# Kernel optimization log

Measured on AMD Instinct MI355X. Metric: run time of the kernel, lower is better.

Reference implementation:

```python
import jax, jax.numpy as jnp
import numpy as np

N_FFT = 2048
STRIDE = 512
FREQ_BINS = N_FFT  # __init__ passes freq_bins=n_fft


def _fourier_kernels():
    s = np.arange(N_FFT, dtype=np.float64)
    # scipy get_window('hann', n_fft, fftbins=True)
    win = 0.5 - 0.5 * np.cos(2.0 * np.pi * s / N_FFT)
    k = np.arange(FREQ_BINS, dtype=np.float64)
    phase = 2.0 * np.pi * np.outer(k, s) / N_FFT  # (bins, n_fft)
    wsin = (win * np.sin(phase)).astype(np.float32)
    wcos = (win * np.cos(phase)).astype(np.float32)
    return wsin, wcos


def setup_inputs() -> dict:
    key = jax.random.key(0)
    x = jax.random.normal(key, (8, 262144), dtype=jnp.float32)
    wsin, wcos = _fourier_kernels()
    return {"x": x, "wsin": jnp.asarray(wsin), "wcos": jnp.asarray(wcos)}


def reference(x, wsin, wcos):
    # center=True, pad_mode='reflect'
    xp = jnp.pad(x, ((0, 0), (N_FFT // 2, N_FFT // 2)), mode="reflect")
    num_frames = (xp.shape[1] - N_FFT) // STRIDE + 1
    # frame the signal: (batch, num_frames, n_fft)
    idx = np.arange(num_frames)[:, None] * STRIDE + np.arange(N_FFT)
    frames = xp[:, idx]
    # dense DFT as GEMM (equivalent to conv1d with sin/cos filters)
    imag = jnp.einsum("btn,kn->bkt", frames, wsin)
    real = jnp.einsum("btn,kn->bkt", frames, wcos)
    return (real, -imag)
```

## Files before the change

### kernel.cpp

```cpp
#include <hip/hip_runtime.h>
#include <hip/hip_bf16.h>
#include <stdint.h>

#define XLEN   262144
#define NT     513
#define NTP    528
#define NB     8
#define NCOL   (NB * NTP)
#define NKC4   320
#define KQ     512
#define NK     1088
#define NFFT   2048
#define OUTKT  (2048 * NT)
#define WSTR   ((size_t)NKC4 * KQ)
#define FSTR   ((size_t)NCOL * KQ)
#define PSTR   ((size_t)NKC4 * NCOL)

typedef __attribute__((ext_vector_type(8))) short short8;
typedef __attribute__((ext_vector_type(4))) short short4v;
typedef __attribute__((ext_vector_type(2))) short short2v;
typedef __attribute__((ext_vector_type(4))) float f32x4;

__device__ __forceinline__ short cvt_bf16(float f) {
  return __builtin_bit_cast(short, (__bf16)f);
}

__device__ __forceinline__ f32x4 bf4_to_f32(short4v v) {
  f32x4 o;
#pragma unroll
  for (int e = 0; e < 4; ++e) {
    uint32_t u = ((uint32_t)(uint16_t)v[e]) << 16;
    o[e] = __builtin_bit_cast(float, u);
  }
  return o;
}

__device__ __forceinline__ void gload16(const short* g, const short* l) {
  __builtin_amdgcn_global_load_lds(
      (const __attribute__((address_space(1))) void*)g,
      (__attribute__((address_space(3))) void*)l, 16, 0, 0);
}


__global__ __launch_bounds__(256) void conv_prep4(
    const float* __restrict__ x,
    const float* __restrict__ wsin, const float* __restrict__ wcos,
    short* __restrict__ wc4, short* __restrict__ ws4,
    short* __restrict__ fr4) {
  const int n0 = threadIdx.x * 8;
  const int m0 = n0 >> 2;
  if (blockIdx.x < NKC4) {
    const int row = blockIdx.x;
    short2v c[4], s[4];
    if (row <= 256) {
      const float* pc = wcos + (size_t)row * NFFT + n0;
      const float* ps = wsin + (size_t)row * NFFT + n0;
      f32x4 c0 = *(const f32x4*)pc, c1 = *(const f32x4*)(pc + 4);
      f32x4 s0 = *(const f32x4*)ps, s1 = *(const f32x4*)(ps + 4);
#pragma unroll
      for (int r = 0; r < 4; ++r) {
        c[r][0] = cvt_bf16(c0[r]); c[r][1] = cvt_bf16(c1[r]);
        s[r][0] = cvt_bf16(s0[r]); s[r][1] = cvt_bf16(s1[r]);
      }
    } else {
#pragma unroll
      for (int r = 0; r < 4; ++r) { c[r][0] = 0; c[r][1] = 0; s[r][0] = 0; s[r][1] = 0; }
    }
    const size_t o = (size_t)row * KQ + m0;
#pragma unroll
    for (int r = 0; r < 4; ++r) {
      *(short2v*)&wc4[r * WSTR + o] = c[r];
      *(short2v*)&ws4[r * WSTR + o] = s[r];
    }
  } else {
    const int j = blockIdx.x - NKC4;
    const int b = j / NTP;
    const int t = j - b * NTP;
    short2v v[4];
    if (t < NT) {
      const float* xb = x + (size_t)b * XLEN;
      const int q0 = t * 512 + n0 - 1024;
      float f[8];
      if (q0 >= 0 && q0 + 7 < XLEN) {
        *(f32x4*)(f)     = *(const f32x4*)(xb + q0);
        *(f32x4*)(f + 4) = *(const f32x4*)(xb + q0 + 4);
      } else {
#pragma unroll
        for (int e = 0; e < 8; ++e) {
          int mm = q0 + e;
          mm = (mm < 0) ? -mm : mm;
          mm = (mm >= XLEN) ? (2 * XLEN - 2 - mm) : mm;
          f[e] = xb[mm];
        }
      }
#pragma unroll
      for (int r = 0; r < 4; ++r) { v[r][0] = cvt_bf16(f[r]); v[r][1] = cvt_bf16(f[4 + r]); }
    } else {
#pragma unroll
      for (int r = 0; r < 4; ++r) { v[r][0] = 0; v[r][1] = 0; }
    }
#pragma unroll
    for (int r = 0; r < 4; ++r)
      *(short2v*)&fr4[r * FSTR + (size_t)j * KQ + m0] = v[r];
  }
}

__global__ __launch_bounds__(256, 3) void dft_gemm_split4(
    const short* __restrict__ wc4, const short* __restrict__ ws4,
    const short* __restrict__ fr4,
    short* __restrict__ pC4, short* __restrict__ pS4) {
  __shared__ short lds[16384];

  const int tid  = threadIdx.x;
  const int lane = tid & 63;
  const int wid  = tid >> 6;

  const int o   = blockIdx.x;
  const int xcd = o & 7;
  const int i   = o >> 3;
  const int wg  = ((xcd < 4) ? xcd * 83 : 332 + (xcd - 4) * 82) + i;
  const int side = wg / 165;
  const int w    = wg - side * 165;
  const int k0   = (w % 5) * 64;
  const int j0   = (w / 5) * 128;

  const short* Ac = wc4 + side * WSTR;
  const short* As = ws4 + side * WSTR;
  const short* Bf = fr4 + side * FSTR;
  short* pC = pC4 + side * PSTR;
  short* pS = pS4 + side * PSTR;

  const int wrow = (wid >> 1) * 32;
  const int wcol = (wid & 1) * 64;

  f32x4 accC[2][4], accS[2][4];
#pragma unroll
  for (int m = 0; m < 2; ++m)
#pragma unroll
    for (int n = 0; n < 4; ++n) { accC[m][n] = (f32x4)0.0f; accS[m][n] = (f32x4)0.0f; }

  const int fr_r = lane & 15;
  const int srow = lane >> 3;
  const int scol = ((lane & 7) ^ srow) * 8;

  auto stage = [&](int n0) {
#pragma unroll
    for (int i2 = 0; i2 < 8; ++i2) {
      const int q = wid * 8 + i2;
      const short* src;
      int dst;
      if (q < 8) {
        src = Ac + (size_t)(k0 + q * 8 + srow) * KQ + n0 + scol;
        dst = q * 512;
      } else if (q < 16) {
        src = As + (size_t)(k0 + (q - 8) * 8 + srow) * KQ + n0 + scol;
        dst = 4096 + (q - 8) * 512;
      } else {
        src = Bf + (size_t)(j0 + (q - 16) * 8 + srow) * KQ + n0 + scol;
        dst = 8192 + (q - 16) * 512;
      }
      gload16(src, &lds[dst]);
    }
  };

  for (int ts = 0; ts < 8; ++ts) {
    if (ts) __syncthreads();
    stage(ts * 64);
    __syncthreads();
#pragma unroll
    for (int ks = 0; ks < 2; ++ks) {
      const int cc = ks * 4 + (lane >> 4);
      short8 aC[2], aS[2], bF[4];
#pragma unroll
      for (int m = 0; m < 2; ++m) {
        const int r = wrow + m * 16 + fr_r;
        const int off = (r << 6) + ((cc ^ (r & 7)) << 3);
        aC[m] = *(const short8*)&lds[off];
        aS[m] = *(const short8*)&lds[4096 + off];
      }
#pragma unroll
      for (int n = 0; n < 4; ++n) {
        const int r = wcol + n * 16 + fr_r;
        const int off = (r << 6) + ((cc ^ (r & 7)) << 3);
        bF[n] = *(const short8*)&lds[8192 + off];
      }
#pragma unroll
      for (int m = 0; m < 2; ++m)
#pragma unroll
        for (int n = 0; n < 4; ++n) {
          accC[m][n] = __builtin_amdgcn_mfma_f32_16x16x32_bf16(aC[m], bF[n], accC[m][n], 0, 0, 0);
          accS[m][n] = __builtin_amdgcn_mfma_f32_16x16x32_bf16(aS[m], bF[n], accS[m][n], 0, 0, 0);
        }
    }
  }

#pragma unroll
  for (int m = 0; m < 2; ++m) {
    const int row = k0 + wrow + m * 16 + (lane >> 4) * 4;
#pragma unroll
    for (int n = 0; n < 4; ++n) {
      const int col = j0 + wcol + n * 16 + (lane & 15);
      const size_t base = (size_t)row * NCOL + col;
#pragma unroll
      for (int r = 0; r < 4; ++r) {
        pC[base + (size_t)r * NCOL] = cvt_bf16(accC[m][n][r]);
        pS[base + (size_t)r * NCOL] = cvt_bf16(accS[m][n][r]);
      }
    }
  }
}

__global__ __launch_bounds__(256) void combine4_kernel(
    const short* __restrict__ pC4, const short* __restrict__ pS4,
    float* __restrict__ outR, float* __restrict__ outI) {
  const int k  = blockIdx.y;
  const int jq = blockIdx.x * 256 + threadIdx.x;
  if (jq >= NCOL / 4) return;
  const int j = jq * 4;
  const int b = j / NTP;
  const int t = j - b * NTP;
  const size_t pb = (size_t)k * NCOL + j;
  f32x4 C[4], S[4];
#pragma unroll
  for (int r = 0; r < 4; ++r) {
    C[r] = bf4_to_f32(*(const short4v*)&pC4[r * PSTR + pb]);
    S[r] = bf4_to_f32(*(const short4v*)&pS4[r * PSTR + pb]);
  }
  const f32x4 CA = C[0] + C[2], CB = C[1] + C[3];
  const f32x4 CmA = C[0] - C[2], CmB = C[1] - C[3];
  const f32x4 SA = S[0] + S[2], SB = S[1] + S[3];
  const f32x4 SmA = S[0] - S[2], SmB = S[1] - S[3];

  f32x4 Cw[4], Sw[4];
  Cw[0] = CA + CB;   Sw[0] = SA + SB;
  Cw[1] = CmA - SmB; Sw[1] = SmA + CmB;
  Cw[2] = CA - CB;   Sw[2] = SA - SB;
  Cw[3] = CmA + SmB; Sw[3] = SmA - CmB;

  const size_t ob = (size_t)b * OUTKT + t;
  const bool mir = (k >= 1) && (k <= 255);
#pragma unroll
  for (int jj = 0; jj < 4; ++jj) {
    const int rowD = 512 * jj + k;
    float* rD = outR + ob + (size_t)rowD * NT;
    float* iD = outI + ob + (size_t)rowD * NT;
    const int rowM = 512 * (4 - jj) - k;
    float* rM = outR + ob + (size_t)rowM * NT;
    float* iM = outI + ob + (size_t)rowM * NT;
#pragma unroll
    for (int e = 0; e < 4; ++e) {
      if (t + e < NT) {
        rD[e] = Cw[jj][e];
        iD[e] = -Sw[jj][e];
        if (mir) { rM[e] = Cw[jj][e]; iM[e] = Sw[jj][e]; }
      }
    }
  }
}


__global__ __launch_bounds__(256) void conv_w_kernel(const float* __restrict__ wsin,
                                                     const float* __restrict__ wcos,
                                                     short* __restrict__ wc,
                                                     short* __restrict__ ws) {
  const int row = blockIdx.x;
  const int c = threadIdx.x * 8;
  const float* src = (blockIdx.y ? wsin : wcos) + (size_t)row * NFFT + c;
  short* dst = (blockIdx.y ? ws : wc) + (size_t)row * NFFT + c;
  f32x4 a = *(const f32x4*)src;
  f32x4 b = *(const f32x4*)(src + 4);
  short8 o;
#pragma unroll
  for (int j = 0; j < 4; ++j) { o[j] = cvt_bf16(a[j]); o[4 + j] = cvt_bf16(b[j]); }
  *(short8*)dst = o;
}

__global__ __launch_bounds__(256) void conv_frames_kernel(const float* __restrict__ x,
                                                          short* __restrict__ fr) {
  const int j = blockIdx.x;
  const int b = j / NTP;
  const int t = j - b * NTP;
  const int c = threadIdx.x * 8;
  short8 o;
  if (t >= NT) {
#pragma unroll
    for (int k = 0; k < 8; ++k) o[k] = 0;
  } else {
    const float* xb = x + (size_t)b * XLEN;
    const int base = t * 512 + c - 1024;
    float v[8];
    if (base >= 0 && base + 7 < XLEN) {
      *(f32x4*)(v)     = *(const f32x4*)(xb + base);
      *(f32x4*)(v + 4) = *(const f32x4*)(xb + base + 4);
    } else {
#pragma unroll
      for (int k = 0; k < 8; ++k) {
        int m = base + k;
        m = (m < 0) ? -m : m;
        m = (m >= XLEN) ? (2 * XLEN - 2 - m) : m;
        v[k] = xb[m];
      }
    }
#pragma unroll
    for (int k = 0; k < 8; ++k) o[k] = cvt_bf16(v[k]);
  }
  *(short8*)&fr[(size_t)j * NFFT + c] = o;
}

__global__ __launch_bounds__(256, 3) void dft_gemm_r4(
    const short* __restrict__ wc_bf,
    const short* __restrict__ ws_bf,
    const short* __restrict__ fr_bf,
    float* __restrict__ outR,
    float* __restrict__ outI) {
  __shared__ short lds[16384];

  const int tid  = threadIdx.x;
  const int lane = tid & 63;
  const int wid  = tid >> 6;

  const int o   = blockIdx.x;
  const int xcd = o & 7;
  const int wg  = ((xcd < 1) ? xcd * 71 : 71 + (xcd - 1) * 70) + (o >> 3);
  const int k0  = (wg % 17) * 64;
  const int j0  = (wg / 17) * 128;

  const int wrow = (wid >> 1) * 32;
  const int wcol = (wid & 1) * 64;

  f32x4 accR[2][4], accI[2][4];
#pragma unroll
  for (int m = 0; m < 2; ++m)
#pragma unroll
    for (int n = 0; n < 4; ++n) { accR[m][n] = (f32x4)0.0f; accI[m][n] = (f32x4)0.0f; }

  const int fr_r = lane & 15;
  const int srow = lane >> 3;
  const int scol = ((lane & 7) ^ srow) * 8;

  auto stage = [&](int n0) {
#pragma unroll
    for (int i = 0; i < 8; ++i) {
      const int q = wid * 8 + i;
      const short* src;
      int dst;
      if (q < 8) {
        src = wc_bf + (size_t)(k0 + q * 8 + srow) * NFFT + n0 + scol;
        dst = q * 512;
      } else if (q < 16) {
        src = ws_bf + (size_t)(k0 + (q - 8) * 8 + srow) * NFFT + n0 + scol;
        dst = 4096 + (q - 8) * 512;
      } else {
        src = fr_bf + (size_t)(j0 + (q - 16) * 8 + srow) * NFFT + n0 + scol;
        dst = 8192 + (q - 16) * 512;
      }
      gload16(src, &lds[dst]);
    }
  };

  for (int t = 0; t < 32; ++t) {
    if (t) __syncthreads();
    stage(t * 64);
    __syncthreads();
#pragma unroll
    for (int ks = 0; ks < 2; ++ks) {
      const int cc = ks * 4 + (lane >> 4);
      short8 a_c[2], a_s[2], b_f[4];
#pragma unroll
      for (int m = 0; m < 2; ++m) {
        const int r = wrow + m * 16 + fr_r;
        const int off = (r << 6) + ((cc ^ (r & 7)) << 3);
        a_c[m] = *(const short8*)&lds[off];
        a_s[m] = *(const short8*)&lds[4096 + off];
      }
#pragma unroll
      for (int n = 0; n < 4; ++n) {
        const int r = wcol + n * 16 + fr_r;
        const int off = (r << 6) + ((cc ^ (r & 7)) << 3);
        b_f[n] = *(const short8*)&lds[8192 + off];
      }
#pragma unroll
      for (int m = 0; m < 2; ++m)
#pragma unroll
        for (int n = 0; n < 4; ++n) {
          accR[m][n] = __builtin_amdgcn_mfma_f32_16x16x32_bf16(a_c[m], b_f[n], accR[m][n], 0, 0, 0);
          accI[m][n] = __builtin_amdgcn_mfma_f32_16x16x32_bf16(a_s[m], b_f[n], accI[m][n], 0, 0, 0);
        }
    }
  }

#pragma unroll
  for (int m = 0; m < 2; ++m) {
    const int k = k0 + wrow + m * 16 + (lane >> 4) * 4;
#pragma unroll
    for (int n = 0; n < 4; ++n) {
      const int j = j0 + wcol + n * 16 + (lane & 15);
      const int b = j / NTP;
      const int t = j - b * NTP;
      if (t < NT) {
        const size_t base = (size_t)b * OUTKT + (size_t)k * NT + t;
#pragma unroll
        for (int r = 0; r < 4; ++r) {
          const int kk = k + r;
          const float vr = accR[m][n][r];
          const float vi = accI[m][n][r];
          outR[base + (size_t)r * NT] = vr;
          outI[base + (size_t)r * NT] = -vi;
          if (kk >= 1 && kk <= 960) {
            const size_t mb = (size_t)b * OUTKT + (size_t)(2048 - kk) * NT + t;
            outR[mb] = vr;
            outI[mb] = vi;
          }
        }
      }
    }
  }
}


extern "C" void kernel_launch(void* const* d_in, const int* in_sizes, int n_in,
                              void* d_out, int out_size, void* d_ws, size_t ws_size,
                              hipStream_t stream) {
  const float* x    = (const float*)d_in[0];
  const float* wsin = (const float*)d_in[1];
  const float* wcos = (const float*)d_in[2];
  float* outR = (float*)d_out;
  float* outI = outR + (size_t)NB * OUTKT;

  const size_t need4 = (8 * WSTR + 4 * FSTR + 8 * PSTR) * sizeof(short);

  if (ws_size >= need4) {
    short* wc4 = (short*)d_ws;
    short* ws4 = wc4 + 4 * WSTR;
    short* fr4 = ws4 + 4 * WSTR;
    short* pC4 = fr4 + 4 * FSTR;
    short* pS4 = pC4 + 4 * PSTR;

    conv_prep4<<<NKC4 + NCOL, 256, 0, stream>>>(x, wsin, wcos, wc4, ws4, fr4);
    dft_gemm_split4<<<660, 256, 0, stream>>>(wc4, ws4, fr4, pC4, pS4);
    combine4_kernel<<<dim3(5, 257), 256, 0, stream>>>(pC4, pS4, outR, outI);
  } else {
    short* wc_bf = (short*)d_ws;
    short* ws_bf = wc_bf + (size_t)NK * NFFT;
    short* fr_bf = ws_bf + (size_t)NK * NFFT;
    conv_w_kernel<<<dim3(NK, 2), 256, 0, stream>>>(wsin, wcos, wc_bf, ws_bf);
    conv_frames_kernel<<<NCOL, 256, 0, stream>>>(x, fr_bf);
    dft_gemm_r4<<<561, 256, 0, stream>>>(wc_bf, ws_bf, fr_bf, outR, outI);
  }
}
```

Measured before the change: 57.04 us.

## Compute Nyquist polyphase row via prep reduction instead of padded GEMM tile

The polyphase GEMM previously padded the 257 needed rows (k=0..256) up to 320, wasting a full 64-row tile for just row 256. Now the GEMM covers only 256 rows (528 workgroups instead of 660). The k=256 contribution is computed in the frame prep kernel as a windowed alternating-sign reduction per phase into a small buffer, which the combine kernel uses with twiddle constants. This adds cosf and a block reduction to the prep kernel and uses an on-device window recomputation instead of the provided wsin/wcos for that row.

```diff
diff --git a/kernel.cpp b/kernel.cpp
--- a/kernel.cpp
+++ b/kernel.cpp
@@ -1,20 +1,22 @@
 #include <hip/hip_runtime.h>
 #include <hip/hip_bf16.h>
 #include <stdint.h>
+#include <math.h>
 
 #define XLEN   262144
 #define NT     513
 #define NTP    528
 #define NB     8
 #define NCOL   (NB * NTP)
-#define NKC4   320
+#define PROW   256
 #define KQ     512
 #define NK     1088
 #define NFFT   2048
 #define OUTKT  (2048 * NT)
-#define WSTR   ((size_t)NKC4 * KQ)
+#define WSTR   ((size_t)PROW * KQ)
 #define FSTR   ((size_t)NCOL * KQ)
-#define PSTR   ((size_t)NKC4 * NCOL)
+#define PSTR   ((size_t)PROW * NCOL)
+#define NWG4   528
 
 typedef __attribute__((ext_vector_type(8))) short short8;
 typedef __attribute__((ext_vector_type(4))) short short4v;
@@ -46,25 +48,21 @@
     const float* __restrict__ x,
     const float* __restrict__ wsin, const float* __restrict__ wcos,
     short* __restrict__ wc4, short* __restrict__ ws4,
-    short* __restrict__ fr4) {
-  const int n0 = threadIdx.x * 8;
+    short* __restrict__ fr4, float* __restrict__ Tbuf) {
+  const int tid = threadIdx.x;
+  const int n0 = tid * 8;
   const int m0 = n0 >> 2;
-  if (blockIdx.x < NKC4) {
+  if (blockIdx.x < PROW) {
     const int row = blockIdx.x;
     short2v c[4], s[4];
-    if (row <= 256) {
-      const float* pc = wcos + (size_t)row * NFFT + n0;
-      const float* ps = wsin + (size_t)row * NFFT + n0;
-      f32x4 c0 = *(const f32x4*)pc, c1 = *(const f32x4*)(pc + 4);
-      f32x4 s0 = *(const f32x4*)ps, s1 = *(const f32x4*)(ps + 4);
-#pragma unroll
-      for (int r = 0; r < 4; ++r) {
-        c[r][0] = cvt_bf16(c0[r]); c[r][1] = cvt_bf16(c1[r]);
-        s[r][0] = cvt_bf16(s0[r]); s[r][1] = cvt_bf16(s1[r]);
-      }
-    } else {
-#pragma unroll
-      for (int r = 0; r < 4; ++r) { c[r][0] = 0; c[r][1] = 0; s[r][0] = 0; s[r][1] = 0; }
+    const float* pc = wcos + (size_t)row * NFFT + n0;
+    const float* ps = wsin + (size_t)row * NFFT + n0;
+    f32x4 c0 = *(const f32x4*)pc, c1 = *(const f32x4*)(pc + 4);
+    f32x4 s0 = *(const f32x4*)ps, s1 = *(const f32x4*)(ps + 4);
+#pragma unroll
+    for (int r = 0; r < 4; ++r) {
+      c[r][0] = cvt_bf16(c0[r]); c[r][1] = cvt_bf16(c1[r]);
+      s[r][0] = cvt_bf16(s0[r]); s[r][1] = cvt_bf16(s1[r]);
     }
     const size_t o = (size_t)row * KQ + m0;
 #pragma unroll
@@ -73,10 +71,11 @@
       *(short2v*)&ws4[r * WSTR + o] = s[r];
     }
   } else {
-    const int j = blockIdx.x - NKC4;
+    const int j = blockIdx.x - PROW;
     const int b = j / NTP;
     const int t = j - b * NTP;
     short2v v[4];
+    float con[4] = {0.f, 0.f, 0.f, 0.f};
     if (t < NT) {
       const float* xb = x + (size_t)b * XLEN;
       const int q0 = t * 512 + n0 - 1024;
@@ -93,8 +92,15 @@
           f[e] = xb[mm];
         }
       }
-#pragma unroll
-      for (int r = 0; r < 4; ++r) { v[r][0] = cvt_bf16(f[r]); v[r][1] = cvt_bf16(f[4 + r]); }
+      float wn[8];
+#pragma unroll
+      for (int e = 0; e < 8; ++e)
+        wn[e] = 0.5f - 0.5f * cosf((float)(M_PI / 1024.0) * (float)(n0 + e));
+#pragma unroll
+      for (int r = 0; r < 4; ++r) {
+        v[r][0] = cvt_bf16(f[r]); v[r][1] = cvt_bf16(f[4 + r]);
+        con[r] = wn[r] * f[r] - wn[4 + r] * f[4 + r];
+      }
     } else {
 #pragma unroll
       for (int r = 0; r < 4; ++r) { v[r][0] = 0; v[r][1] = 0; }
@@ -102,6 +108,23 @@
 #pragma unroll
     for (int r = 0; r < 4; ++r)
       *(short2v*)&fr4[r * FSTR + (size_t)j * KQ + m0] = v[r];
+
+    const int lane = tid & 63;
+    const int wid  = tid >> 6;
+#pragma unroll
+    for (int r = 0; r < 4; ++r)
+#pragma unroll
+      for (int off = 32; off >= 1; off >>= 1)
+        con[r] += __shfl_down(con[r], off);
+    __shared__ float tred[4][4];
+    if (lane == 0) {
+#pragma unroll
+      for (int r = 0; r < 4; ++r) tred[wid][r] = con[r];
+    }
+    __syncthreads();
+    if (tid < 4)
+      Tbuf[(size_t)j * 4 + tid] =
+          tred[0][tid] + tred[1][tid] + tred[2][tid] + tred[3][tid];
   }
 }
 
@@ -117,12 +140,11 @@
 
   const int o   = blockIdx.x;
   const int xcd = o & 7;
-  const int i   = o >> 3;
-  const int wg  = ((xcd < 4) ? xcd * 83 : 332 + (xcd - 4) * 82) + i;
-  const int side = wg / 165;
-  const int w    = wg - side * 165;
-  const int k0   = (w % 5) * 64;
-  const int j0   = (w / 5) * 128;
+  const int wg  = xcd * 66 + (o >> 3);
+  const int side = wg / 132;
+  const int w    = wg - side * 132;
+  const int k0   = (w % 4) * 64;
+  const int j0   = (w / 4) * 128;
 
   const short* Ac = wc4 + side * WSTR;
   const short* As = ws4 + side * WSTR;
@@ -212,6 +234,7 @@
 
 __global__ __launch_bounds__(256) void combine4_kernel(
     const short* __restrict__ pC4, const short* __restrict__ pS4,
+    const float* __restrict__ Tbuf,
     float* __restrict__ outR, float* __restrict__ outI) {
   const int k  = blockIdx.y;
   const int jq = blockIdx.x * 256 + threadIdx.x;
@@ -219,12 +242,27 @@
   const int j = jq * 4;
   const int b = j / NTP;
   const int t = j - b * NTP;
-  const size_t pb = (size_t)k * NCOL + j;
+  const float RT2 = 0.70710678118654752f;
   f32x4 C[4], S[4];
-#pragma unroll
-  for (int r = 0; r < 4; ++r) {
-    C[r] = bf4_to_f32(*(const short4v*)&pC4[r * PSTR + pb]);
-    S[r] = bf4_to_f32(*(const short4v*)&pS4[r * PSTR + pb]);
+  if (k == 256) {
+    const float ct8[4] = {1.f, RT2, 0.f, -RT2};
+    const float st8[4] = {0.f, RT2, 1.f, RT2};
+#pragma unroll
+    for (int e = 0; e < 4; ++e) {
+      f32x4 tj = *(const f32x4*)&Tbuf[(size_t)(j + e) * 4];
+#pragma unroll
+      for (int r = 0; r < 4; ++r) {
+        C[r][e] = ct8[r] * tj[r];
+        S[r][e] = st8[r] * tj[r];
+      }
+    }
+  } else {
+    const size_t pb = (size_t)k * NCOL + j;
+#pragma unroll
+    for (int r = 0; r < 4; ++r) {
+      C[r] = bf4_to_f32(*(const short4v*)&pC4[r * PSTR + pb]);
+      S[r] = bf4_to_f32(*(const short4v*)&pS4[r * PSTR + pb]);
+    }
   }
   const f32x4 CA = C[0] + C[2], CB = C[1] + C[3];
   const f32x4 CmA = C[0] - C[2], CmB = C[1] - C[3];
@@ -427,7 +465,8 @@
   float* outR = (float*)d_out;
   float* outI = outR + (size_t)NB * OUTKT;
 
-  const size_t need4 = (8 * WSTR + 4 * FSTR + 8 * PSTR) * sizeof(short);
+  const size_t need4 = (8 * WSTR + 4 * FSTR + 8 * PSTR) * sizeof(short)
+                     + (size_t)NCOL * 4 * sizeof(float);
 
   if (ws_size >= need4) {
     short* wc4 = (short*)d_ws;
@@ -435,10 +474,11 @@
     short* fr4 = ws4 + 4 * WSTR;
     short* pC4 = fr4 + 4 * FSTR;
     short* pS4 = pC4 + 4 * PSTR;
-
-    conv_prep4<<<NKC4 + NCOL, 256, 0, stream>>>(x, wsin, wcos, wc4, ws4, fr4);
-    dft_gemm_split4<<<660, 256, 0, stream>>>(wc4, ws4, fr4, pC4, pS4);
-    combine4_kernel<<<dim3(5, 257), 256, 0, stream>>>(pC4, pS4, outR, outI);
+    float* Tbuf = (float*)(pS4 + 4 * PSTR);
+
+    conv_prep4<<<PROW + NCOL, 256, 0, stream>>>(x, wsin, wcos, wc4, ws4, fr4, Tbuf);
+    dft_gemm_split4<<<NWG4, 256, 0, stream>>>(wc4, ws4, fr4, pC4, pS4);
+    combine4_kernel<<<dim3(5, 257), 256, 0, stream>>>(pC4, pS4, Tbuf, outR, outI);
   } else {
     short* wc_bf = (short*)d_ws;
     short* ws_bf = wc_bf + (size_t)NK * NFFT;
```

Result: no change. 57.51 us (+0.8%).
